# Optimization experiments

Hardware: AMD Instinct MI355X
Metric: run time of the kernel (lower is better)

## Reference

```python
import jax, jax.numpy as jnp
import numpy as np

# ---- constant lookup tables (mirror SoftALU registered buffers) ----
def _build_tables():
    n = np.arange(16)
    A, Bq, C = np.meshgrid(n, n, np.arange(2), indexing='ij')
    total = A + Bq + C
    eye16 = np.eye(16, dtype=np.float32)
    eye2 = np.eye(2, dtype=np.float32)
    add_t = eye16[total % 16]        # (16,16,2,16)
    carry_t = eye2[total // 16]      # (16,16,2,2)
    and_t = eye16[n[:, None] & n[None, :]]
    or_t = eye16[n[:, None] | n[None, :]]
    xor_t = eye16[n[:, None] ^ n[None, :]]
    bb = np.arange(256)
    b2n = np.zeros((256, 32), np.float32)
    b2n[bb, bb >> 4] = 1.0
    b2n[bb, 16 + (bb & 15)] = 1.0
    return tuple(jnp.asarray(t) for t in (add_t, carry_t, and_t, or_t, xor_t, b2n, b2n.T))

ADD_T, CARRY_T, AND_T, OR_T, XOR_T, B2N, N2B = _build_tables()
_SHIFTS = jnp.arange(4, dtype=jnp.uint32) * jnp.uint32(8)
SHARP = 100.0  # softmax sharpening temperature from the original module


def _sharp(x):
    return jax.nn.softmax(SHARP * x, axis=-1)


def _to_nibbles(x):  # x: (B,4,256) -> (high, low) each (B,4,16)
    comb = jnp.einsum('bnc,cm->bnm', x, B2N)
    return _sharp(comb[..., :16]), _sharp(comb[..., 16:])


def _from_nibbles(high, low):  # (...,16),(...,16) -> (...,256)
    return _sharp(jnp.einsum('...m,mc->...c', jnp.concatenate([high, low], axis=-1), N2B))


def _nibble_add(a, b, cin):  # (B,16),(B,16),(B,2) -> sum (B,16), carry (B,2)
    w = jnp.einsum('bi,bj,bk->bijk', a, b, cin)
    s = jnp.einsum('bijk,ijkl->bl', w, ADD_T)
    c = jnp.einsum('bijk,ijkl->bl', w, CARRY_T)
    return _sharp(s), _sharp(c)


def soft_add(a, b):  # (B,4,256) x2 -> (B,4,256), little-endian ripple-carry over 8 nibbles
    ah, al = _to_nibbles(a)
    bh, bl = _to_nibbles(b)
    carry = jnp.broadcast_to(jnp.array([1.0, 0.0], dtype=a.dtype), (a.shape[0], 2))
    out = []
    for i in range(4):  # fixed 4-byte carry recurrence (structural, not data dim)
        s_lo, carry = _nibble_add(al[:, i], bl[:, i], carry)
        s_hi, carry = _nibble_add(ah[:, i], bh[:, i], carry)
        out.append(_from_nibbles(s_hi, s_lo))
    return jnp.stack(out, axis=1)


def soft_bitwise(a, b, table):
    ah, al = _to_nibbles(a)
    bh, bl = _to_nibbles(b)
    r_hi = _sharp(jnp.einsum('bni,bnj,ijk->bnk', ah, bh, table))
    r_lo = _sharp(jnp.einsum('bni,bnj,ijk->bnk', al, bl, table))
    return _from_nibbles(r_hi, r_lo)


def _encode_u32(v):  # (B,) uint32 -> (B,4,256) one-hot bytes (little-endian)
    bytes_ = (v[:, None] >> _SHIFTS) & jnp.uint32(255)
    return jax.nn.one_hot(bytes_, 256, dtype=jnp.float32)


def _decode_u32(x):  # (B,4,256) -> (B,) uint32 (argmax decode, as in module.decode)
    bytes_ = jnp.argmax(x, axis=-1).astype(jnp.uint32)
    return (bytes_ << _SHIFTS).sum(axis=-1).astype(jnp.uint32)


def soft_negate(x):  # two's complement: xor with 0xFF per byte, then +1
    xh, xl = _to_nibbles(x)
    xf = XOR_T[:, 15, :]  # xor-with-0xF map (0xF is an exact one-hot in the original)
    f_hi = _sharp(jnp.einsum('bni,ik->bnk', xh, xf))
    f_lo = _sharp(jnp.einsum('bni,ik->bnk', xl, xf))
    flipped = _from_nibbles(f_hi, f_lo)
    one = _encode_u32(jnp.ones((x.shape[0],), dtype=jnp.uint32))
    return soft_add(flipped, one)


def soft_mul(a, b):
    # Original: decode -> silu(a)*b + silu(-a)*(-b) == exact a*b -> round -> encode.
    # Exact integer product mod 2^32 (encode masks to 32 bits).
    return _encode_u32(_decode_u32(a) * _decode_u32(b))


def soft_div(a, b):
    # decode() yields unsigned 0..2^32-1, so the original's repeated-subtraction
    # loop computes unsigned integer division, with b==0 -> 0.
    av, bv = _decode_u32(a), _decode_u32(b)
    q = jnp.where(bv == jnp.uint32(0), jnp.uint32(0), av // jnp.maximum(bv, jnp.uint32(1)))
    return _encode_u32(q)


def setup_inputs() -> dict:
    key = jax.random.key(0)
    k1, k2 = jax.random.split(key)
    Bsz = 8192
    a = jax.nn.one_hot(jax.random.randint(k1, (Bsz, 4), 0, 256), 256, dtype=jnp.float32)
    b = jax.nn.one_hot(jax.random.randint(k2, (Bsz, 4), 0, 256), 256, dtype=jnp.float32)
    return {"a": a, "b": b}


def reference(a, b):
    # all_ops(): (add, sub, mul, div, and, or, xor) each (B,4,256) -> (7,B,4,256)
    return jnp.stack([
        soft_add(a, b),
        soft_add(a, soft_negate(b)),  # subtract = a + (~b + 1)
        soft_mul(a, b),
        soft_div(a, b),
        soft_bitwise(a, b, AND_T),
        soft_bitwise(a, b, OR_T),
        soft_bitwise(a, b, XOR_T),
    ], axis=0)
```

## Files before the change

kernel.cpp:

```cpp
#include <hip/hip_runtime.h>
#include <stdint.h>


typedef float vfloat4 __attribute__((ext_vector_type(4)));

__global__ __launch_bounds__(256) void softalu_fused(const float* __restrict__ a,
                                                     const float* __restrict__ b,
                                                     vfloat4* __restrict__ out,
                                                     int B) {
    const int batch = blockIdx.x;
    const int t = threadIdx.x;

    __shared__ uint32_t sh_bytes[8];
    __shared__ uint32_t res7[7];

    const vfloat4* a4 = (const vfloat4*)a + (size_t)batch * 256;
    const vfloat4* b4 = (const vfloat4*)b + (size_t)batch * 256;
    const vfloat4 va = a4[t];
    const vfloat4 vb = b4[t];

    const int n = t >> 6;
    const int c0 = (t & 63) * 4;

    if (va.x > 0.5f) sh_bytes[n] = (uint32_t)(c0 + 0);
    if (va.y > 0.5f) sh_bytes[n] = (uint32_t)(c0 + 1);
    if (va.z > 0.5f) sh_bytes[n] = (uint32_t)(c0 + 2);
    if (va.w > 0.5f) sh_bytes[n] = (uint32_t)(c0 + 3);
    if (vb.x > 0.5f) sh_bytes[4 + n] = (uint32_t)(c0 + 0);
    if (vb.y > 0.5f) sh_bytes[4 + n] = (uint32_t)(c0 + 1);
    if (vb.z > 0.5f) sh_bytes[4 + n] = (uint32_t)(c0 + 2);
    if (vb.w > 0.5f) sh_bytes[4 + n] = (uint32_t)(c0 + 3);
    __syncthreads();

    if (t == 0) {
        const uint32_t av = sh_bytes[0] | (sh_bytes[1] << 8) | (sh_bytes[2] << 16) | (sh_bytes[3] << 24);
        const uint32_t bv = sh_bytes[4] | (sh_bytes[5] << 8) | (sh_bytes[6] << 16) | (sh_bytes[7] << 24);
        res7[0] = av + bv;
        res7[1] = av - bv;
        res7[2] = av * bv;
        res7[3] = bv ? (av / bv) : 0u;
        res7[4] = av & bv;
        res7[5] = av | bv;
        res7[6] = av ^ bv;
    }
    __syncthreads();

#pragma unroll
    for (int op = 0; op < 7; ++op) {
        const uint32_t r = res7[op];
        const int rb = (int)((r >> (8 * n)) & 255u);
        vfloat4 v;
        v.x = (c0 + 0 == rb) ? 1.0f : 0.0f;
        v.y = (c0 + 1 == rb) ? 1.0f : 0.0f;
        v.z = (c0 + 2 == rb) ? 1.0f : 0.0f;
        v.w = (c0 + 3 == rb) ? 1.0f : 0.0f;
        __builtin_nontemporal_store(v, &out[((size_t)op * B + batch) * 256 + t]);
    }
}

extern "C" void kernel_launch(void* const* d_in, const int* in_sizes, int n_in,
                              void* d_out, int out_size, void* d_ws, size_t ws_size,
                              hipStream_t stream) {
    const float* a = (const float*)d_in[0];
    const float* b = (const float*)d_in[1];
    const int B = in_sizes[0] / (4 * 256);
    (void)d_ws; (void)ws_size;
    softalu_fused<<<B, 256, 0, stream>>>(a, b, (vfloat4*)d_out, B);
}
```

Measured before the change: 287.5 us.

## Process one batch element per wavefront using ballot/readlane instead of LDS and barriers

Each 64-lane wavefront now handles a whole batch element: it loops over the 4 bytes, finds the hot index with a ballot plus readlane, and computes all seven results redundantly in every lane. This removes the shared-memory staging, both block barriers, and the single-thread serial section. Four batch elements are packed per block. In exchange each lane issues four times as many loads and stores, and the wave-level reductions add a few instructions.

Result: faster. 276.7 us (median of 2 runs) (-3.8%).

```diff
diff --git a/kernel.cpp b/kernel.cpp
--- a/kernel.cpp
+++ b/kernel.cpp
@@ -4,57 +4,70 @@
 
 typedef float vfloat4 __attribute__((ext_vector_type(4)));
 
-__global__ __launch_bounds__(256) void softalu_fused(const float* __restrict__ a,
-                                                     const float* __restrict__ b,
-                                                     vfloat4* __restrict__ out,
-                                                     int B) {
-    const int batch = blockIdx.x;
-    const int t = threadIdx.x;
-
-    __shared__ uint32_t sh_bytes[8];
-    __shared__ uint32_t res7[7];
+__global__ __launch_bounds__(256) void softalu_wave(const float* __restrict__ a,
+                                                    const float* __restrict__ b,
+                                                    vfloat4* __restrict__ out,
+                                                    int B) {
+    const int wave_in_blk = threadIdx.x >> 6;
+    const int lane = threadIdx.x & 63;
+    const int batch = blockIdx.x * 4 + wave_in_blk;
+    if (batch >= B) return;
 
     const vfloat4* a4 = (const vfloat4*)a + (size_t)batch * 256;
     const vfloat4* b4 = (const vfloat4*)b + (size_t)batch * 256;
-    const vfloat4 va = a4[t];
-    const vfloat4 vb = b4[t];
 
-    const int n = t >> 6;
-    const int c0 = (t & 63) * 4;
+    uint32_t av = 0u, bv = 0u;
+#pragma unroll
+    for (int n = 0; n < 4; ++n) {
+        const vfloat4 va = a4[n * 64 + lane];
+        const vfloat4 vb = b4[n * 64 + lane];
 
-    if (va.x > 0.5f) sh_bytes[n] = (uint32_t)(c0 + 0);
-    if (va.y > 0.5f) sh_bytes[n] = (uint32_t)(c0 + 1);
-    if (va.z > 0.5f) sh_bytes[n] = (uint32_t)(c0 + 2);
-    if (va.w > 0.5f) sh_bytes[n] = (uint32_t)(c0 + 3);
-    if (vb.x > 0.5f) sh_bytes[4 + n] = (uint32_t)(c0 + 0);
-    if (vb.y > 0.5f) sh_bytes[4 + n] = (uint32_t)(c0 + 1);
-    if (vb.z > 0.5f) sh_bytes[4 + n] = (uint32_t)(c0 + 2);
-    if (vb.w > 0.5f) sh_bytes[4 + n] = (uint32_t)(c0 + 3);
-    __syncthreads();
+        int ca = 0;
+        bool ha = false;
+        if (va.x > 0.5f) { ha = true; ca = lane * 4 + 0; }
+        if (va.y > 0.5f) { ha = true; ca = lane * 4 + 1; }
+        if (va.z > 0.5f) { ha = true; ca = lane * 4 + 2; }
+        if (va.w > 0.5f) { ha = true; ca = lane * 4 + 3; }
 
-    if (t == 0) {
-        const uint32_t av = sh_bytes[0] | (sh_bytes[1] << 8) | (sh_bytes[2] << 16) | (sh_bytes[3] << 24);
-        const uint32_t bv = sh_bytes[4] | (sh_bytes[5] << 8) | (sh_bytes[6] << 16) | (sh_bytes[7] << 24);
-        res7[0] = av + bv;
-        res7[1] = av - bv;
-        res7[2] = av * bv;
-        res7[3] = bv ? (av / bv) : 0u;
-        res7[4] = av & bv;
-        res7[5] = av | bv;
-        res7[6] = av ^ bv;
+        int cb = 0;
+        bool hb = false;
+        if (vb.x > 0.5f) { hb = true; cb = lane * 4 + 0; }
+        if (vb.y > 0.5f) { hb = true; cb = lane * 4 + 1; }
+        if (vb.z > 0.5f) { hb = true; cb = lane * 4 + 2; }
+        if (vb.w > 0.5f) { hb = true; cb = lane * 4 + 3; }
+
+        const unsigned long long ma = __ballot(ha);
+        const unsigned long long mb = __ballot(hb);
+        const int La = __ffsll((unsigned long long)ma) - 1;
+        const int Lb = __ffsll((unsigned long long)mb) - 1;
+        av |= ((uint32_t)__builtin_amdgcn_readlane(ca, La)) << (8 * n);
+        bv |= ((uint32_t)__builtin_amdgcn_readlane(cb, Lb)) << (8 * n);
     }
-    __syncthreads();
 
+    uint32_t res[7];
+    res[0] = av + bv;
+    res[1] = av - bv;
+    res[2] = av * bv;
+    res[3] = bv ? (av / bv) : 0u;
+    res[4] = av & bv;
+    res[5] = av | bv;
+    res[6] = av ^ bv;
+
+    const int c0 = lane * 4;
 #pragma unroll
     for (int op = 0; op < 7; ++op) {
-        const uint32_t r = res7[op];
-        const int rb = (int)((r >> (8 * n)) & 255u);
-        vfloat4 v;
-        v.x = (c0 + 0 == rb) ? 1.0f : 0.0f;
-        v.y = (c0 + 1 == rb) ? 1.0f : 0.0f;
-        v.z = (c0 + 2 == rb) ? 1.0f : 0.0f;
-        v.w = (c0 + 3 == rb) ? 1.0f : 0.0f;
-        __builtin_nontemporal_store(v, &out[((size_t)op * B + batch) * 256 + t]);
+        const uint32_t r = res[op];
+        vfloat4* orow = out + ((size_t)op * B + batch) * 256;
+#pragma unroll
+        for (int n = 0; n < 4; ++n) {
+            const int rb = (int)((r >> (8 * n)) & 255u);
+            vfloat4 v;
+            v.x = (c0 + 0 == rb) ? 1.0f : 0.0f;
+            v.y = (c0 + 1 == rb) ? 1.0f : 0.0f;
+            v.z = (c0 + 2 == rb) ? 1.0f : 0.0f;
+            v.w = (c0 + 3 == rb) ? 1.0f : 0.0f;
+            __builtin_nontemporal_store(v, &orow[n * 64 + lane]);
+        }
     }
 }
 
@@ -65,5 +78,5 @@
     const float* b = (const float*)d_in[1];
     const int B = in_sizes[0] / (4 * 256);
     (void)d_ws; (void)ws_size;
-    softalu_fused<<<B, 256, 0, stream>>>(a, b, (vfloat4*)d_out, B);
+    softalu_wave<<<(B + 3) / 4, 256, 0, stream>>>(a, b, (vfloat4*)d_out, B);
 }
```
